# Performance work log

Measured on AMD Instinct MI355X. Metric: run time of the kernel, lower is better.

Reference implementation:

```python
import jax, jax.numpy as jnp
import numpy as np

BLOCK = 64
# Standard NF4 codebook (bitsandbytes), 16 quantile-based values in [-1, 1].
NF4_CODEBOOK = jnp.array([
    -1.0, -0.6961928009986877, -0.5250730514526367, -0.39491748809814453,
    -0.28444138169288635, -0.18477343022823334, -0.09105003625154495, 0.0,
    0.07958029955625534, 0.16093020141124725, 0.24611230194568634,
    0.33791524171829224, 0.44070982933044434, 0.5626170039176941,
    0.6848514676094055, 1.0], dtype=jnp.float32)


def dequantize_nf4(codes, absmax, shape):
    # codes: int array of 4-bit indices (unpacked), absmax: one scale per BLOCK.
    vals = NF4_CODEBOOK[codes.reshape(-1)]              # [N]
    vals = vals.reshape(-1, BLOCK) * absmax[:, None]    # blockwise rescale
    return vals.reshape(shape)


def setup_inputs() -> dict:
    key = jax.random.key(0)
    k1, k2, k3, k4, k5 = jax.random.split(key, 5)
    B, S, D_IN, D_OUT = 4, 2048, 4096, 4096
    x = jax.random.normal(k1, (B, S, D_IN), dtype=jnp.float32)
    w_codes = jax.random.randint(k2, (D_OUT, D_IN), 0, 16, dtype=jnp.int32)
    w_absmax = jax.random.uniform(k3, (D_OUT * D_IN // BLOCK,), dtype=jnp.float32)
    b_codes = jax.random.randint(k4, (D_OUT,), 0, 16, dtype=jnp.int32)
    b_absmax = jax.random.uniform(k5, (D_OUT // BLOCK,), dtype=jnp.float32)
    return {"x": x, "w_codes": w_codes, "w_absmax": w_absmax,
            "b_codes": b_codes, "b_absmax": b_absmax}


def reference(x, w_codes, w_absmax, b_codes, b_absmax):
    W = dequantize_nf4(w_codes, w_absmax, w_codes.shape)   # [out, in]
    b = dequantize_nf4(b_codes, b_absmax, b_codes.shape)   # [out]
    # F.linear(x, W, b) = x @ W.T + b
    return jnp.einsum('bsd,od->bso', x, W) + b
```

## Files before the change

kernel.cpp:

```cpp
#include <hip/hip_runtime.h>
#include <stdint.h>

typedef __bf16 bf16_t;
typedef __attribute__((ext_vector_type(8))) __bf16 bf16x8;
typedef __attribute__((ext_vector_type(4))) float f32x4;
typedef __attribute__((ext_vector_type(8))) unsigned short ushort8;
typedef __attribute__((ext_vector_type(4))) int int4v;
typedef __attribute__((ext_vector_type(4))) float float4v;

typedef const void __attribute__((address_space(1)))* gptr_t;
typedef void __attribute__((address_space(3)))* lptr_t;

__constant__ float NF4_CB[16] = {
    -1.0f, -0.6961928009986877f, -0.5250730514526367f, -0.39491748809814453f,
    -0.28444138169288635f, -0.18477343022823334f, -0.09105003625154495f, 0.0f,
    0.07958029955625534f, 0.16093020141124725f, 0.24611230194568634f,
    0.33791524171829224f, 0.44070982933044434f, 0.5626170039176941f,
    0.6848514676094055f, 1.0f};

__device__ __forceinline__ unsigned short f32_to_bf16_rne(float f) {
    unsigned int u = __float_as_uint(f);
    u += 0x7FFFu + ((u >> 16) & 1u);
    return (unsigned short)(u >> 16);
}

__global__ void dequant_w_kernel(const int* __restrict__ codes,
                                 const float* __restrict__ absmax,
                                 unsigned short* __restrict__ out, long n8) {
    long t = (long)blockIdx.x * blockDim.x + threadIdx.x;
    if (t >= n8) return;
    long base = t * 8;
    float am = absmax[t >> 3];
    int4v c0 = *(const int4v*)(codes + base);
    int4v c1 = *(const int4v*)(codes + base + 4);
    ushort8 v;
    v[0] = f32_to_bf16_rne(NF4_CB[c0[0]] * am);
    v[1] = f32_to_bf16_rne(NF4_CB[c0[1]] * am);
    v[2] = f32_to_bf16_rne(NF4_CB[c0[2]] * am);
    v[3] = f32_to_bf16_rne(NF4_CB[c0[3]] * am);
    v[4] = f32_to_bf16_rne(NF4_CB[c1[0]] * am);
    v[5] = f32_to_bf16_rne(NF4_CB[c1[1]] * am);
    v[6] = f32_to_bf16_rne(NF4_CB[c1[2]] * am);
    v[7] = f32_to_bf16_rne(NF4_CB[c1[3]] * am);
    *(ushort8*)(out + base) = v;
}

__global__ void cvt_x_kernel(const float* __restrict__ x,
                             unsigned short* __restrict__ out, long n8) {
    long t = (long)blockIdx.x * blockDim.x + threadIdx.x;
    if (t >= n8) return;
    long base = t * 8;
    float4v f0 = *(const float4v*)(x + base);
    float4v f1 = *(const float4v*)(x + base + 4);
    ushort8 v;
    v[0] = f32_to_bf16_rne(f0[0]);
    v[1] = f32_to_bf16_rne(f0[1]);
    v[2] = f32_to_bf16_rne(f0[2]);
    v[3] = f32_to_bf16_rne(f0[3]);
    v[4] = f32_to_bf16_rne(f1[0]);
    v[5] = f32_to_bf16_rne(f1[1]);
    v[6] = f32_to_bf16_rne(f1[2]);
    v[7] = f32_to_bf16_rne(f1[3]);
    *(ushort8*)(out + base) = v;
}

__global__ void bias_kernel(const int* __restrict__ bc,
                            const float* __restrict__ bam,
                            float* __restrict__ bias, int n) {
    int o = blockIdx.x * blockDim.x + threadIdx.x;
    if (o >= n) return;
    bias[o] = NF4_CB[bc[o]] * bam[o >> 6];
}

__global__ void gemm_bias_kernel(const bf16_t* __restrict__ A,
                                 const bf16_t* __restrict__ B,
                                 const float* __restrict__ bias,
                                 float* __restrict__ C,
                                 int M, int N, int K) {
    __shared__ __align__(16) bf16_t sAB[8192];

    const int t = threadIdx.x;
    const int lane = t & 63;
    const int wave = t >> 6;
    const int tileM = blockIdx.y * 128;
    const int tileN = blockIdx.x * 128;

    const bf16_t* src[4];
    bf16_t* ldst[4];
#pragma unroll
    for (int j = 0; j < 4; ++j) {
        int chunk = wave * 4 + j;
        int r = (chunk & 7) * 16 + (lane >> 2);
        int kk = (lane & 3) * 8;
        const bf16_t* base = (chunk < 8) ? (A + (size_t)(tileM + r) * K)
                                         : (B + (size_t)(tileN + r) * K);
        src[j] = base + kk;
        ldst[j] = &sAB[chunk * 512 + lane * 8];
    }

    const int wm = wave >> 1;
    const int wn = wave & 1;
    const int aoff = (wm * 64 + (lane & 15)) * 32 + (lane >> 4) * 8;
    const int boff = 4096 + (wn * 64 + (lane & 15)) * 32 + (lane >> 4) * 8;

    f32x4 acc[4][4] = {};

    for (int kt = 0; kt < K; kt += 32) {
#pragma unroll
        for (int j = 0; j < 4; ++j) {
            __builtin_amdgcn_global_load_lds((gptr_t)(src[j]), (lptr_t)(ldst[j]),
                                             16, 0, 0);
            src[j] += 32;
        }
        __syncthreads();

        bf16x8 a[4], b[4];
#pragma unroll
        for (int i = 0; i < 4; ++i) a[i] = *(const bf16x8*)&sAB[aoff + i * 512];
#pragma unroll
        for (int i = 0; i < 4; ++i) b[i] = *(const bf16x8*)&sAB[boff + i * 512];
#pragma unroll
        for (int mi = 0; mi < 4; ++mi)
#pragma unroll
            for (int ni = 0; ni < 4; ++ni)
                acc[mi][ni] = __builtin_amdgcn_mfma_f32_16x16x32_bf16(
                    a[mi], b[ni], acc[mi][ni], 0, 0, 0);
        __syncthreads();
    }

    const int col0 = tileN + wn * 64 + (lane & 15);
    const int row0 = tileM + wm * 64 + (lane >> 4) * 4;
    float bv[4];
#pragma unroll
    for (int ni = 0; ni < 4; ++ni) bv[ni] = bias[col0 + ni * 16];
#pragma unroll
    for (int mi = 0; mi < 4; ++mi)
#pragma unroll
        for (int ni = 0; ni < 4; ++ni)
#pragma unroll
            for (int r = 0; r < 4; ++r)
                C[(size_t)(row0 + mi * 16 + r) * N + (col0 + ni * 16)] =
                    acc[mi][ni][r] + bv[ni];
}

extern "C" void kernel_launch(void* const* d_in, const int* in_sizes, int n_in,
                              void* d_out, int out_size, void* d_ws, size_t ws_size,
                              hipStream_t stream) {
    const float* x        = (const float*)d_in[0];
    const int*   w_codes  = (const int*)d_in[1];
    const float* w_absmax = (const float*)d_in[2];
    const int*   b_codes  = (const int*)d_in[3];
    const float* b_absmax = (const float*)d_in[4];
    float* out = (float*)d_out;

    const int  D_OUT = in_sizes[3];
    const long WK    = (long)in_sizes[1];
    const int  D_IN  = (int)(WK / D_OUT);
    const long xN    = (long)in_sizes[0];
    const int  M     = (int)(xN / D_IN);
    const int  N = D_OUT, K = D_IN;

    unsigned short* wsW = (unsigned short*)d_ws;
    unsigned short* wsA = wsW + (size_t)N * K;
    float* wsBias = (float*)(wsA + (size_t)M * K);

    long w8 = WK / 8;
    dequant_w_kernel<<<dim3((unsigned)((w8 + 255) / 256)), dim3(256), 0, stream>>>(
        w_codes, w_absmax, wsW, w8);

    long x8 = xN / 8;
    cvt_x_kernel<<<dim3((unsigned)((x8 + 255) / 256)), dim3(256), 0, stream>>>(
        x, wsA, x8);

    bias_kernel<<<dim3((N + 255) / 256), dim3(256), 0, stream>>>(
        b_codes, b_absmax, wsBias, N);

    gemm_bias_kernel<<<dim3(N / 128, M / 128), dim3(256), 0, stream>>>(
        (const bf16_t*)wsA, (const bf16_t*)wsW, wsBias, out, M, N, K);
}
```

Before: 575.3 us.

## Merge prep kernels and double GEMM K-step with XOR-swizzled LDS layout

```diff
diff --git a/kernel.cpp b/kernel.cpp
--- a/kernel.cpp
+++ b/kernel.cpp
@@ -24,52 +24,54 @@
     return (unsigned short)(u >> 16);
 }
 
-__global__ void dequant_w_kernel(const int* __restrict__ codes,
-                                 const float* __restrict__ absmax,
-                                 unsigned short* __restrict__ out, long n8) {
-    long t = (long)blockIdx.x * blockDim.x + threadIdx.x;
-    if (t >= n8) return;
-    long base = t * 8;
-    float am = absmax[t >> 3];
-    int4v c0 = *(const int4v*)(codes + base);
-    int4v c1 = *(const int4v*)(codes + base + 4);
-    ushort8 v;
-    v[0] = f32_to_bf16_rne(NF4_CB[c0[0]] * am);
-    v[1] = f32_to_bf16_rne(NF4_CB[c0[1]] * am);
-    v[2] = f32_to_bf16_rne(NF4_CB[c0[2]] * am);
-    v[3] = f32_to_bf16_rne(NF4_CB[c0[3]] * am);
-    v[4] = f32_to_bf16_rne(NF4_CB[c1[0]] * am);
-    v[5] = f32_to_bf16_rne(NF4_CB[c1[1]] * am);
-    v[6] = f32_to_bf16_rne(NF4_CB[c1[2]] * am);
-    v[7] = f32_to_bf16_rne(NF4_CB[c1[3]] * am);
-    *(ushort8*)(out + base) = v;
-}
-
-__global__ void cvt_x_kernel(const float* __restrict__ x,
-                             unsigned short* __restrict__ out, long n8) {
-    long t = (long)blockIdx.x * blockDim.x + threadIdx.x;
-    if (t >= n8) return;
-    long base = t * 8;
-    float4v f0 = *(const float4v*)(x + base);
-    float4v f1 = *(const float4v*)(x + base + 4);
-    ushort8 v;
-    v[0] = f32_to_bf16_rne(f0[0]);
-    v[1] = f32_to_bf16_rne(f0[1]);
-    v[2] = f32_to_bf16_rne(f0[2]);
-    v[3] = f32_to_bf16_rne(f0[3]);
-    v[4] = f32_to_bf16_rne(f1[0]);
-    v[5] = f32_to_bf16_rne(f1[1]);
-    v[6] = f32_to_bf16_rne(f1[2]);
-    v[7] = f32_to_bf16_rne(f1[3]);
-    *(ushort8*)(out + base) = v;
-}
-
-__global__ void bias_kernel(const int* __restrict__ bc,
-                            const float* __restrict__ bam,
-                            float* __restrict__ bias, int n) {
-    int o = blockIdx.x * blockDim.x + threadIdx.x;
-    if (o >= n) return;
-    bias[o] = NF4_CB[bc[o]] * bam[o >> 6];
+__global__ void prep_kernel(const int* __restrict__ w_codes,
+                            const float* __restrict__ w_absmax,
+                            const float* __restrict__ x,
+                            const int* __restrict__ b_codes,
+                            const float* __restrict__ b_absmax,
+                            unsigned short* __restrict__ outW,
+                            unsigned short* __restrict__ outA,
+                            float* __restrict__ outBias,
+                            long w8, long x8, int nbias, long wb, long xb) {
+    long blk = blockIdx.x;
+    if (blk < wb) {
+        long t = blk * blockDim.x + threadIdx.x;
+        if (t >= w8) return;
+        long base = t * 8;
+        float am = w_absmax[t >> 3];
+        int4v c0 = *(const int4v*)(w_codes + base);
+        int4v c1 = *(const int4v*)(w_codes + base + 4);
+        ushort8 v;
+        v[0] = f32_to_bf16_rne(NF4_CB[c0[0]] * am);
+        v[1] = f32_to_bf16_rne(NF4_CB[c0[1]] * am);
+        v[2] = f32_to_bf16_rne(NF4_CB[c0[2]] * am);
+        v[3] = f32_to_bf16_rne(NF4_CB[c0[3]] * am);
+        v[4] = f32_to_bf16_rne(NF4_CB[c1[0]] * am);
+        v[5] = f32_to_bf16_rne(NF4_CB[c1[1]] * am);
+        v[6] = f32_to_bf16_rne(NF4_CB[c1[2]] * am);
+        v[7] = f32_to_bf16_rne(NF4_CB[c1[3]] * am);
+        *(ushort8*)(outW + base) = v;
+    } else if (blk < wb + xb) {
+        long t = (blk - wb) * blockDim.x + threadIdx.x;
+        if (t >= x8) return;
+        long base = t * 8;
+        float4v f0 = *(const float4v*)(x + base);
+        float4v f1 = *(const float4v*)(x + base + 4);
+        ushort8 v;
+        v[0] = f32_to_bf16_rne(f0[0]);
+        v[1] = f32_to_bf16_rne(f0[1]);
+        v[2] = f32_to_bf16_rne(f0[2]);
+        v[3] = f32_to_bf16_rne(f0[3]);
+        v[4] = f32_to_bf16_rne(f1[0]);
+        v[5] = f32_to_bf16_rne(f1[1]);
+        v[6] = f32_to_bf16_rne(f1[2]);
+        v[7] = f32_to_bf16_rne(f1[3]);
+        *(ushort8*)(outA + base) = v;
+    } else {
+        int o = (int)(blk - wb - xb) * blockDim.x + threadIdx.x;
+        if (o >= nbias) return;
+        outBias[o] = NF4_CB[b_codes[o]] * b_absmax[o >> 6];
+    }
 }
 
 __global__ void gemm_bias_kernel(const bf16_t* __restrict__ A,
@@ -77,7 +79,7 @@
                                  const float* __restrict__ bias,
                                  float* __restrict__ C,
                                  int M, int N, int K) {
-    __shared__ __align__(16) bf16_t sAB[8192];
+    __shared__ __align__(16) bf16_t sAB[16384];
 
     const int t = threadIdx.x;
     const int lane = t & 63;
@@ -85,51 +87,55 @@
     const int tileM = blockIdx.y * 128;
     const int tileN = blockIdx.x * 128;
 
-    const bf16_t* src[4];
-    bf16_t* ldst[4];
-#pragma unroll
-    for (int j = 0; j < 4; ++j) {
-        int chunk = wave * 4 + j;
-        int r = (chunk & 7) * 16 + (lane >> 2);
-        int kk = (lane & 3) * 8;
-        const bf16_t* base = (chunk < 8) ? (A + (size_t)(tileM + r) * K)
-                                         : (B + (size_t)(tileN + r) * K);
-        src[j] = base + kk;
-        ldst[j] = &sAB[chunk * 512 + lane * 8];
-    }
+    const int rloc = lane >> 3;
+    const int jsw  = (lane & 7) ^ rloc;
+    const int chunk0 = wave * 8;
+    const int isB = chunk0 >> 4;
+    const int ci0 = chunk0 & 15;
+    const int r0 = ci0 * 8 + rloc;
+    const bf16_t* srcp = (isB ? (B + (size_t)(tileN + r0) * K)
+                              : (A + (size_t)(tileM + r0) * K)) + jsw * 8;
+    bf16_t* dstp = &sAB[isB * 8192 + ci0 * 512 + lane * 8];
+    const size_t srcChunkStride = (size_t)8 * K;
 
     const int wm = wave >> 1;
     const int wn = wave & 1;
-    const int aoff = (wm * 64 + (lane & 15)) * 32 + (lane >> 4) * 8;
-    const int boff = 4096 + (wn * 64 + (lane & 15)) * 32 + (lane >> 4) * 8;
+    const int la = lane & 15;
+    const int jA = lane >> 4;
+    const int jj0 = (jA ^ (lane & 7)) * 8;
+    const int aoff = (wm * 64 + la) * 64 + jj0;
+    const int boff = 8192 + (wn * 64 + la) * 64 + jj0;
 
     f32x4 acc[4][4] = {};
 
-    for (int kt = 0; kt < K; kt += 32) {
+    for (int kt = 0; kt < K; kt += 64) {
 #pragma unroll
-        for (int j = 0; j < 4; ++j) {
-            __builtin_amdgcn_global_load_lds((gptr_t)(src[j]), (lptr_t)(ldst[j]),
-                                             16, 0, 0);
-            src[j] += 32;
-        }
+        for (int j8 = 0; j8 < 8; ++j8)
+            __builtin_amdgcn_global_load_lds((gptr_t)(srcp + j8 * srcChunkStride),
+                                             (lptr_t)(dstp + j8 * 512), 16, 0, 0);
+        srcp += 64;
         __syncthreads();
 
-        bf16x8 a[4], b[4];
 #pragma unroll
-        for (int i = 0; i < 4; ++i) a[i] = *(const bf16x8*)&sAB[aoff + i * 512];
+        for (int kh = 0; kh < 2; ++kh) {
+            const int kx = kh * 32;
+            bf16x8 a[4], b[4];
 #pragma unroll
-        for (int i = 0; i < 4; ++i) b[i] = *(const bf16x8*)&sAB[boff + i * 512];
+            for (int i = 0; i < 4; ++i) a[i] = *(const bf16x8*)&sAB[(aoff + i * 1024) ^ kx];
 #pragma unroll
-        for (int mi = 0; mi < 4; ++mi)
+            for (int i = 0; i < 4; ++i) b[i] = *(const bf16x8*)&sAB[(boff + i * 1024) ^ kx];
 #pragma unroll
-            for (int ni = 0; ni < 4; ++ni)
-                acc[mi][ni] = __builtin_amdgcn_mfma_f32_16x16x32_bf16(
-                    a[mi], b[ni], acc[mi][ni], 0, 0, 0);
+            for (int mi = 0; mi < 4; ++mi)
+#pragma unroll
+                for (int ni = 0; ni < 4; ++ni)
+                    acc[mi][ni] = __builtin_amdgcn_mfma_f32_16x16x32_bf16(
+                        a[mi], b[ni], acc[mi][ni], 0, 0, 0);
+        }
         __syncthreads();
     }
 
-    const int col0 = tileN + wn * 64 + (lane & 15);
-    const int row0 = tileM + wm * 64 + (lane >> 4) * 4;
+    const int col0 = tileN + wn * 64 + la;
+    const int row0 = tileM + wm * 64 + jA * 4;
     float bv[4];
 #pragma unroll
     for (int ni = 0; ni < 4; ++ni) bv[ni] = bias[col0 + ni * 16];
@@ -165,15 +171,13 @@
     float* wsBias = (float*)(wsA + (size_t)M * K);
 
     long w8 = WK / 8;
-    dequant_w_kernel<<<dim3((unsigned)((w8 + 255) / 256)), dim3(256), 0, stream>>>(
-        w_codes, w_absmax, wsW, w8);
-
     long x8 = xN / 8;
-    cvt_x_kernel<<<dim3((unsigned)((x8 + 255) / 256)), dim3(256), 0, stream>>>(
-        x, wsA, x8);
-
-    bias_kernel<<<dim3((N + 255) / 256), dim3(256), 0, stream>>>(
-        b_codes, b_absmax, wsBias, N);
+    long wb = (w8 + 255) / 256;
+    long xb = (x8 + 255) / 256;
+    long bb = (D_OUT + 255) / 256;
+    prep_kernel<<<dim3((unsigned)(wb + xb + bb)), dim3(256), 0, stream>>>(
+        w_codes, w_absmax, x, b_codes, b_absmax, wsW, wsA, wsBias,
+        w8, x8, D_OUT, wb, xb);
 
     gemm_bias_kernel<<<dim3(N / 128, M / 128), dim3(256), 0, stream>>>(
         (const bf16_t*)wsA, (const bf16_t*)wsW, wsBias, out, M, N, K);
```

Result: faster. 522.5 us (-9.2%).
